# Kernel tuning notes

Measured on AMD Instinct MI355X. Metric: run time of the kernel, lower is better.

## Reference

```python
import jax, jax.numpy as jnp
import numpy as np

N_NODES = 100000
IN_DIM = 256
HIDDEN = 512
N_INC = 1000000   # incidence (gather/scatter) list length
N_SEG = 100000    # number of hyperedges / segments


def setup_inputs() -> dict:
    key = jax.random.key(0)
    ks = jax.random.split(key, 6)
    x = jax.random.normal(ks[0], (N_NODES, IN_DIM), dtype=jnp.float32)
    target_nodes = jax.random.randint(ks[1], (N_INC,), 0, N_NODES, dtype=jnp.int32)
    target_ids = jnp.sort(jax.random.randint(ks[2], (N_INC,), 0, N_SEG, dtype=jnp.int32))
    # Linear params (PyTorch stores [out,in]; we keep [in,out] and matmul directly)
    W1 = jax.random.normal(ks[3], (IN_DIM, HIDDEN), dtype=jnp.float32) * (1.0 / np.sqrt(IN_DIM))
    b1 = jnp.zeros((HIDDEN,), dtype=jnp.float32)
    W2 = jax.random.normal(ks[4], (HIDDEN, 1), dtype=jnp.float32) * (1.0 / np.sqrt(HIDDEN))
    b2 = jnp.zeros((1,), dtype=jnp.float32)
    return {"x": x, "target_nodes": target_nodes, "target_ids": target_ids,
            "num_segments": N_SEG, "W1": W1, "b1": b1, "W2": W2, "b2": b2}


def reference(x, target_nodes, target_ids, num_segments, W1, b1, W2, b2):
    # gather node features, scatter-sum into segments (hyperedges)
    gathered = x[target_nodes, :]                                   # [N_INC, IN_DIM]
    Z = jax.ops.segment_sum(gathered, target_ids,
                            num_segments=num_segments)              # [N_SEG, IN_DIM]
    Z = jnp.maximum(Z @ W1 + b1, 0.0)                               # linear + relu
    # dropout is identity in eval mode
    Z = Z @ W2 + b2                                                 # [N_SEG, 1]
    return jax.nn.sigmoid(Z)[:, 0]                                  # squeeze(-1)
```

## Files before the change

kernel.cpp:

```cpp
#include <hip/hip_runtime.h>
#include <hip/hip_bf16.h>
#include <math.h>

#define N_NODES   100000
#define IN_DIM    256
#define HIDDEN    512
#define N_INC     1000000
#define N_SEG     100000

typedef __attribute__((ext_vector_type(8))) short bf16x8;
typedef __attribute__((ext_vector_type(4))) float f32x4;

__device__ __forceinline__ unsigned short f2bf(float f) {
  unsigned int u = __builtin_bit_cast(unsigned int, f);
  u += 0x7FFFu + ((u >> 16) & 1u);
  return (unsigned short)(u >> 16);
}
__device__ __forceinline__ float bflo(unsigned int u) {
  return __builtin_bit_cast(float, u << 16);
}
__device__ __forceinline__ float bfhi(unsigned int u) {
  return __builtin_bit_cast(float, u & 0xFFFF0000u);
}

__global__ void k_seg_starts(const int* __restrict__ ids, int* __restrict__ starts) {
  int s = blockIdx.x * blockDim.x + threadIdx.x;
  if (s > N_SEG) return;
  int lo = 0, hi = N_INC;
  while (lo < hi) {
    int mid = (lo + hi) >> 1;
    if (ids[mid] < s) lo = mid + 1; else hi = mid;
  }
  starts[s] = lo;
}

__global__ void k_w1t(const float* __restrict__ W1, unsigned short* __restrict__ W1t) {
  int idx = blockIdx.x * 256 + threadIdx.x;
  int k  = idx >> 7;
  int c4 = idx & 127;
  float4 v = *(const float4*)(W1 + (size_t)k * HIDDEN + c4 * 4);
  W1t[(c4 * 4 + 0) * IN_DIM + k] = f2bf(v.x);
  W1t[(c4 * 4 + 1) * IN_DIM + k] = f2bf(v.y);
  W1t[(c4 * 4 + 2) * IN_DIM + k] = f2bf(v.z);
  W1t[(c4 * 4 + 3) * IN_DIM + k] = f2bf(v.w);
}

__global__ void k_xbf(const float* __restrict__ x, unsigned short* __restrict__ xb) {
  size_t idx = (size_t)blockIdx.x * 256 + threadIdx.x;
  float4 v = *(const float4*)(x + idx * 4);
  uint2 p;
  p.x = (unsigned)f2bf(v.x) | ((unsigned)f2bf(v.y) << 16);
  p.y = (unsigned)f2bf(v.z) | ((unsigned)f2bf(v.w) << 16);
  *(uint2*)(xb + idx * 4) = p;
}

__global__ void k_segsum(const unsigned short* __restrict__ xb, const int* __restrict__ nodes,
                         const int* __restrict__ starts, unsigned short* __restrict__ Zb) {
  int wave = threadIdx.x >> 6;
  int lane = threadIdx.x & 63;
  int s = blockIdx.x * 4 + wave;
  if (s >= N_SEG) return;
  int beg = starts[s];
  int end = starts[s + 1];
  float a0 = 0.f, a1 = 0.f, a2 = 0.f, a3 = 0.f;
  int j = beg;
  for (; j + 3 < end; j += 4) {
    int n0 = nodes[j], n1 = nodes[j + 1], n2 = nodes[j + 2], n3 = nodes[j + 3];
    uint2 v0 = *(const uint2*)(xb + (size_t)n0 * IN_DIM + lane * 4);
    uint2 v1 = *(const uint2*)(xb + (size_t)n1 * IN_DIM + lane * 4);
    uint2 v2 = *(const uint2*)(xb + (size_t)n2 * IN_DIM + lane * 4);
    uint2 v3 = *(const uint2*)(xb + (size_t)n3 * IN_DIM + lane * 4);
    a0 += bflo(v0.x) + bflo(v1.x) + bflo(v2.x) + bflo(v3.x);
    a1 += bfhi(v0.x) + bfhi(v1.x) + bfhi(v2.x) + bfhi(v3.x);
    a2 += bflo(v0.y) + bflo(v1.y) + bflo(v2.y) + bflo(v3.y);
    a3 += bfhi(v0.y) + bfhi(v1.y) + bfhi(v2.y) + bfhi(v3.y);
  }
  for (; j < end; ++j) {
    int n0 = nodes[j];
    uint2 v0 = *(const uint2*)(xb + (size_t)n0 * IN_DIM + lane * 4);
    a0 += bflo(v0.x); a1 += bfhi(v0.x); a2 += bflo(v0.y); a3 += bfhi(v0.y);
  }
  uint2 p;
  p.x = (unsigned)f2bf(a0) | ((unsigned)f2bf(a1) << 16);
  p.y = (unsigned)f2bf(a2) | ((unsigned)f2bf(a3) << 16);
  *(uint2*)(Zb + (size_t)s * IN_DIM + lane * 4) = p;
}

__global__ __launch_bounds__(256, 2) void k_mlp(
    const unsigned short* __restrict__ Zb, const unsigned short* __restrict__ W1t,
    const float* __restrict__ b1, const float* __restrict__ W2,
    const float* __restrict__ b2, float* __restrict__ out) {
  __shared__ __align__(16) unsigned short Bf[8][64][8];
  const int tid  = threadIdx.x;
  const int wave = tid >> 6;
  const int lane = tid & 63;
  const int m0   = blockIdx.x * 128 + wave * 32;

  uint4 a[2][8];
  const int arow = m0 + (lane & 15);
  const int ak   = (lane >> 4) * 8;
  #pragma unroll
  for (int kc = 0; kc < 8; ++kc) {
    #pragma unroll
    for (int rf = 0; rf < 2; ++rf) {
      int row = arow + rf * 16;
      if (row < N_NODES)
        a[rf][kc] = *(const uint4*)(Zb + (size_t)row * IN_DIM + kc * 32 + ak);
      else
        a[rf][kc] = make_uint4(0u, 0u, 0u, 0u);
    }
  }

  float logit[2][4];
  #pragma unroll
  for (int rf = 0; rf < 2; ++rf)
    #pragma unroll
    for (int e = 0; e < 4; ++e) logit[rf][e] = 0.f;

  for (int nt = 0; nt < 4; ++nt) {
    const int c0 = nt * 128;
    f32x4 acc[2][8];
    #pragma unroll
    for (int rf = 0; rf < 2; ++rf)
      #pragma unroll
      for (int cf = 0; cf < 8; ++cf) acc[rf][cf] = (f32x4){0.f, 0.f, 0.f, 0.f};

    for (int kc = 0; kc < 8; ++kc) {
      #pragma unroll
      for (int it = 0; it < 2; ++it) {
        int idx  = it * 256 + tid;
        int frag = idx >> 6;
        int l2   = idx & 63;
        int col  = c0 + frag * 16 + (l2 & 15);
        int kk   = kc * 32 + (l2 >> 4) * 8;
        *(uint4*)&Bf[frag][l2][0] = *(const uint4*)(W1t + col * IN_DIM + kk);
      }
      __syncthreads();
      bf16x8 av0 = __builtin_bit_cast(bf16x8, a[0][kc]);
      bf16x8 av1 = __builtin_bit_cast(bf16x8, a[1][kc]);
      #pragma unroll
      for (int cf = 0; cf < 8; ++cf) {
        bf16x8 bv = *(const bf16x8*)&Bf[cf][lane][0];
        acc[0][cf] = __builtin_amdgcn_mfma_f32_16x16x32_bf16(av0, bv, acc[0][cf], 0, 0, 0);
        acc[1][cf] = __builtin_amdgcn_mfma_f32_16x16x32_bf16(av1, bv, acc[1][cf], 0, 0, 0);
      }
      __syncthreads();
    }
    #pragma unroll
    for (int cf = 0; cf < 8; ++cf) {
      int c = c0 + cf * 16 + (lane & 15);
      float bb = b1[c];
      float w2 = W2[c];
      #pragma unroll
      for (int rf = 0; rf < 2; ++rf)
        #pragma unroll
        for (int e = 0; e < 4; ++e) {
          float h = acc[rf][cf][e] + bb;
          h = h > 0.f ? h : 0.f;
          logit[rf][e] = fmaf(h, w2, logit[rf][e]);
        }
    }
  }
  #pragma unroll
  for (int rf = 0; rf < 2; ++rf)
    #pragma unroll
    for (int e = 0; e < 4; ++e) {
      float v = logit[rf][e];
      v += __shfl_xor(v, 1, 64);
      v += __shfl_xor(v, 2, 64);
      v += __shfl_xor(v, 4, 64);
      v += __shfl_xor(v, 8, 64);
      logit[rf][e] = v;
    }
  if ((lane & 15) == 0) {
    float bb2 = b2[0];
    #pragma unroll
    for (int rf = 0; rf < 2; ++rf)
      #pragma unroll
      for (int e = 0; e < 4; ++e) {
        int row = m0 + rf * 16 + (lane >> 4) * 4 + e;
        if (row < N_NODES)
          out[row] = 1.f / (1.f + expf(-(logit[rf][e] + bb2)));
      }
  }
}

extern "C" void kernel_launch(void* const* d_in, const int* in_sizes, int n_in,
                              void* d_out, int out_size, void* d_ws, size_t ws_size,
                              hipStream_t stream) {
  const float* x   = (const float*)d_in[0];
  const int* nodes = (const int*)d_in[1];
  const int* ids   = (const int*)d_in[2];
  const float* W1  = (const float*)d_in[4];
  const float* b1  = (const float*)d_in[5];
  const float* W2  = (const float*)d_in[6];
  const float* b2  = (const float*)d_in[7];
  float* out       = (float*)d_out;

  char* ws = (char*)d_ws;
  int* starts = (int*)ws;
  size_t off = (((size_t)(N_SEG + 1) * sizeof(int)) + 1023) & ~(size_t)1023;
  unsigned short* Zb = (unsigned short*)(ws + off);
  off += (size_t)N_NODES * IN_DIM * sizeof(unsigned short);
  off = (off + 1023) & ~(size_t)1023;
  unsigned short* W1t = (unsigned short*)(ws + off);
  off += (size_t)HIDDEN * IN_DIM * sizeof(unsigned short);
  off = (off + 1023) & ~(size_t)1023;
  unsigned short* xb = (unsigned short*)(ws + off);

  k_seg_starts<<<(N_SEG + 1 + 255) / 256, 256, 0, stream>>>(ids, starts);
  k_w1t<<<128, 256, 0, stream>>>(W1, W1t);
  k_xbf<<<(N_NODES * IN_DIM / 4) / 256 + 1, 256, 0, stream>>>(x, xb);
  k_segsum<<<(N_SEG + 3) / 4, 256, 0, stream>>>(xb, nodes, starts, Zb);
  k_mlp<<<(N_NODES + 127) / 128, 256, 0, stream>>>(Zb, W1t, b1, W2, b2, out);
}
```

Baseline: 169.4 us.

## Widen segsum gathers to 16B with half-wave split; stage two K-chunks per barrier

The segment-sum kernel now has each half-wave handle alternate incidence entries with 16-byte loads per lane, so a wave holds more gathers in flight. The two halves are combined with a cross-half shuffle before the store. The MLP kernel stages two K-chunks of W1 into shared memory per barrier pair, halving the number of __syncthreads. Costs are doubled LDS use per block and some extra shuffles.

```diff
diff --git a/kernel.cpp b/kernel.cpp
--- a/kernel.cpp
+++ b/kernel.cpp
@@ -21,6 +21,9 @@
 }
 __device__ __forceinline__ float bfhi(unsigned int u) {
   return __builtin_bit_cast(float, u & 0xFFFF0000u);
+}
+__device__ __forceinline__ unsigned pack2(float a, float b) {
+  return (unsigned)f2bf(a) | ((unsigned)f2bf(b) << 16);
 }
 
 __global__ void k_seg_starts(const int* __restrict__ ids, int* __restrict__ starts) {
@@ -49,10 +52,16 @@
   size_t idx = (size_t)blockIdx.x * 256 + threadIdx.x;
   float4 v = *(const float4*)(x + idx * 4);
   uint2 p;
-  p.x = (unsigned)f2bf(v.x) | ((unsigned)f2bf(v.y) << 16);
-  p.y = (unsigned)f2bf(v.z) | ((unsigned)f2bf(v.w) << 16);
+  p.x = pack2(v.x, v.y);
+  p.y = pack2(v.z, v.w);
   *(uint2*)(xb + idx * 4) = p;
 }
+
+#define ACC8(v)                                                        \
+  acc0 += bflo((v).x); acc1 += bfhi((v).x);                            \
+  acc2 += bflo((v).y); acc3 += bfhi((v).y);                            \
+  acc4 += bflo((v).z); acc5 += bfhi((v).z);                            \
+  acc6 += bflo((v).w); acc7 += bfhi((v).w);
 
 __global__ void k_segsum(const unsigned short* __restrict__ xb, const int* __restrict__ nodes,
                          const int* __restrict__ starts, unsigned short* __restrict__ Zb) {
@@ -60,37 +69,50 @@
   int lane = threadIdx.x & 63;
   int s = blockIdx.x * 4 + wave;
   if (s >= N_SEG) return;
-  int beg = starts[s];
-  int end = starts[s + 1];
-  float a0 = 0.f, a1 = 0.f, a2 = 0.f, a3 = 0.f;
-  int j = beg;
-  for (; j + 3 < end; j += 4) {
-    int n0 = nodes[j], n1 = nodes[j + 1], n2 = nodes[j + 2], n3 = nodes[j + 3];
-    uint2 v0 = *(const uint2*)(xb + (size_t)n0 * IN_DIM + lane * 4);
-    uint2 v1 = *(const uint2*)(xb + (size_t)n1 * IN_DIM + lane * 4);
-    uint2 v2 = *(const uint2*)(xb + (size_t)n2 * IN_DIM + lane * 4);
-    uint2 v3 = *(const uint2*)(xb + (size_t)n3 * IN_DIM + lane * 4);
-    a0 += bflo(v0.x) + bflo(v1.x) + bflo(v2.x) + bflo(v3.x);
-    a1 += bfhi(v0.x) + bfhi(v1.x) + bfhi(v2.x) + bfhi(v3.x);
-    a2 += bflo(v0.y) + bflo(v1.y) + bflo(v2.y) + bflo(v3.y);
-    a3 += bfhi(v0.y) + bfhi(v1.y) + bfhi(v2.y) + bfhi(v3.y);
-  }
-  for (; j < end; ++j) {
+  const int beg = starts[s];
+  const int end = starts[s + 1];
+  const int half = lane >> 5;
+  const int sl   = lane & 31;
+  const unsigned short* base = xb + sl * 8;
+  float acc0 = 0.f, acc1 = 0.f, acc2 = 0.f, acc3 = 0.f;
+  float acc4 = 0.f, acc5 = 0.f, acc6 = 0.f, acc7 = 0.f;
+  int j = beg + half;
+  for (; j + 6 < end; j += 8) {
+    int n0 = nodes[j], n1 = nodes[j + 2], n2 = nodes[j + 4], n3 = nodes[j + 6];
+    uint4 v0 = *(const uint4*)(base + (size_t)n0 * IN_DIM);
+    uint4 v1 = *(const uint4*)(base + (size_t)n1 * IN_DIM);
+    uint4 v2 = *(const uint4*)(base + (size_t)n2 * IN_DIM);
+    uint4 v3 = *(const uint4*)(base + (size_t)n3 * IN_DIM);
+    ACC8(v0); ACC8(v1); ACC8(v2); ACC8(v3);
+  }
+  for (; j < end; j += 2) {
     int n0 = nodes[j];
-    uint2 v0 = *(const uint2*)(xb + (size_t)n0 * IN_DIM + lane * 4);
-    a0 += bflo(v0.x); a1 += bfhi(v0.x); a2 += bflo(v0.y); a3 += bfhi(v0.y);
-  }
-  uint2 p;
-  p.x = (unsigned)f2bf(a0) | ((unsigned)f2bf(a1) << 16);
-  p.y = (unsigned)f2bf(a2) | ((unsigned)f2bf(a3) << 16);
-  *(uint2*)(Zb + (size_t)s * IN_DIM + lane * 4) = p;
+    uint4 v0 = *(const uint4*)(base + (size_t)n0 * IN_DIM);
+    ACC8(v0);
+  }
+  acc0 += __shfl_xor(acc0, 32, 64);
+  acc1 += __shfl_xor(acc1, 32, 64);
+  acc2 += __shfl_xor(acc2, 32, 64);
+  acc3 += __shfl_xor(acc3, 32, 64);
+  acc4 += __shfl_xor(acc4, 32, 64);
+  acc5 += __shfl_xor(acc5, 32, 64);
+  acc6 += __shfl_xor(acc6, 32, 64);
+  acc7 += __shfl_xor(acc7, 32, 64);
+  if (half == 0) {
+    uint4 p;
+    p.x = pack2(acc0, acc1);
+    p.y = pack2(acc2, acc3);
+    p.z = pack2(acc4, acc5);
+    p.w = pack2(acc6, acc7);
+    *(uint4*)(Zb + (size_t)s * IN_DIM + sl * 8) = p;
+  }
 }
 
 __global__ __launch_bounds__(256, 2) void k_mlp(
     const unsigned short* __restrict__ Zb, const unsigned short* __restrict__ W1t,
     const float* __restrict__ b1, const float* __restrict__ W2,
     const float* __restrict__ b2, float* __restrict__ out) {
-  __shared__ __align__(16) unsigned short Bf[8][64][8];
+  __shared__ __align__(16) unsigned short Bf[2][8][64][8];
   const int tid  = threadIdx.x;
   const int wave = tid >> 6;
   const int lane = tid & 63;
@@ -125,24 +147,30 @@
       #pragma unroll
       for (int cf = 0; cf < 8; ++cf) acc[rf][cf] = (f32x4){0.f, 0.f, 0.f, 0.f};
 
-    for (int kc = 0; kc < 8; ++kc) {
-      #pragma unroll
-      for (int it = 0; it < 2; ++it) {
+    for (int ks = 0; ks < 4; ++ks) {
+      #pragma unroll
+      for (int it = 0; it < 4; ++it) {
         int idx  = it * 256 + tid;
-        int frag = idx >> 6;
-        int l2   = idx & 63;
+        int sub  = idx >> 9;
+        int rem  = idx & 511;
+        int frag = rem >> 6;
+        int l2   = rem & 63;
         int col  = c0 + frag * 16 + (l2 & 15);
-        int kk   = kc * 32 + (l2 >> 4) * 8;
-        *(uint4*)&Bf[frag][l2][0] = *(const uint4*)(W1t + col * IN_DIM + kk);
+        int kk   = (ks * 2 + sub) * 32 + (l2 >> 4) * 8;
+        *(uint4*)&Bf[sub][frag][l2][0] = *(const uint4*)(W1t + col * IN_DIM + kk);
       }
       __syncthreads();
-      bf16x8 av0 = __builtin_bit_cast(bf16x8, a[0][kc]);
-      bf16x8 av1 = __builtin_bit_cast(bf16x8, a[1][kc]);
-      #pragma unroll
-      for (int cf = 0; cf < 8; ++cf) {
-        bf16x8 bv = *(const bf16x8*)&Bf[cf][lane][0];
-        acc[0][cf] = __builtin_amdgcn_mfma_f32_16x16x32_bf16(av0, bv, acc[0][cf], 0, 0, 0);
-        acc[1][cf] = __builtin_amdgcn_mfma_f32_16x16x32_bf16(av1, bv, acc[1][cf], 0, 0, 0);
+      #pragma unroll
+      for (int sub = 0; sub < 2; ++sub) {
+        int kc = ks * 2 + sub;
+        bf16x8 av0 = __builtin_bit_cast(bf16x8, a[0][kc]);
+        bf16x8 av1 = __builtin_bit_cast(bf16x8, a[1][kc]);
+        #pragma unroll
+        for (int cf = 0; cf < 8; ++cf) {
+          bf16x8 bv = *(const bf16x8*)&Bf[sub][cf][lane][0];
+          acc[0][cf] = __builtin_amdgcn_mfma_f32_16x16x32_bf16(av0, bv, acc[0][cf], 0, 0, 0);
+          acc[1][cf] = __builtin_amdgcn_mfma_f32_16x16x32_bf16(av1, bv, acc[1][cf], 0, 0, 0);
+        }
       }
       __syncthreads();
     }
```

New measurement: 164.2 us. 1.03x faster.
